# Optimization experiments

Measured on AMD Instinct MI355X. Metric: run time of the kernel, lower is better.

The kernel has to match this reference:

```python
import jax, jax.numpy as jnp
import numpy as np


def setup_inputs() -> dict:
    key = jax.random.key(0)
    kx, ks = jax.random.split(key)
    M, N, D = 8192, 8192, 512
    X = jax.random.normal(kx, (M, D), dtype=jnp.float32)
    svs = jax.random.normal(ks, (N, D), dtype=jnp.float32)
    # scale = 1/(2*sigma^2); a plausible fitted value for standard-normal data
    scale = jnp.asarray(0.01, dtype=jnp.float32)
    return {"X": X, "svs": svs, "scale": scale}


def reference(X, svs, scale):
    N, D = svs.shape
    x2 = jnp.sum(X * X, axis=-1, keepdims=True)          # [M, 1]
    s2 = jnp.sum(svs * svs, axis=-1)                      # [N]
    dist2 = x2 + s2[None, :] - 2.0 * (X @ svs.T)          # [M, N]
    dist2 = jnp.maximum(dist2, 0.0)
    log_p = (jax.scipy.special.logsumexp(-scale * dist2, axis=-1)
             - jnp.log(jnp.asarray(N, dtype=X.dtype))
             + (D / 2) * jnp.log(scale / jnp.pi))
    return log_p
```

## Files before the change

kernel.cpp:

```cpp
#include <hip/hip_runtime.h>
#include <hip/hip_bf16.h>
#include <hip/hip_fp8.h>
#include <math.h>

typedef __attribute__((ext_vector_type(4))) int   int4v;
typedef __attribute__((ext_vector_type(8))) int   int8v;
typedef __attribute__((ext_vector_type(4))) float f32x4;

#define AS1 __attribute__((address_space(1)))
#define AS3 __attribute__((address_space(3)))

__global__ __launch_bounds__(256) void prep_kernel(
    const float* __restrict__ X, const float* __restrict__ S,
    unsigned char* __restrict__ Xq, unsigned char* __restrict__ Sq,
    float* __restrict__ x2, float* __restrict__ s2,
    float* __restrict__ rowsum, int M, int R, int Dv)
{
    const int gid  = blockIdx.x * 256 + threadIdx.x;
    const int nthr = gridDim.x * 256;

    for (int i = gid; i < M; i += nthr) rowsum[i] = 0.f;

    const int lane = threadIdx.x & 63;
    const int wid  = gid >> 6;
    const int nw   = nthr >> 6;

    for (int row = wid; row < R; row += nw) {
        const float* rp;
        unsigned char* op;
        float* sq;
        if (row < M) { rp = X + (size_t)row * Dv;       op = Xq + (size_t)row * Dv;       sq = x2 + row; }
        else         { rp = S + (size_t)(row - M) * Dv; op = Sq + (size_t)(row - M) * Dv; sq = s2 + (row - M); }

        float acc = 0.f;
        for (int k = lane * 8; k < Dv; k += 64 * 8) {
            float4 v0 = *(const float4*)(rp + k);
            float4 v1 = *(const float4*)(rp + k + 4);
            acc += v0.x * v0.x + v0.y * v0.y + v0.z * v0.z + v0.w * v0.w;
            acc += v1.x * v1.x + v1.y * v1.y + v1.z * v1.z + v1.w * v1.w;
            union { __hip_fp8_e4m3 h[8]; uint2 u; } pk;
            pk.h[0] = __hip_fp8_e4m3(v0.x);
            pk.h[1] = __hip_fp8_e4m3(v0.y);
            pk.h[2] = __hip_fp8_e4m3(v0.z);
            pk.h[3] = __hip_fp8_e4m3(v0.w);
            pk.h[4] = __hip_fp8_e4m3(v1.x);
            pk.h[5] = __hip_fp8_e4m3(v1.y);
            pk.h[6] = __hip_fp8_e4m3(v1.z);
            pk.h[7] = __hip_fp8_e4m3(v1.w);
            *(uint2*)(op + k) = pk.u;
        }
#pragma unroll
        for (int off = 1; off < 64; off <<= 1)
            acc += __shfl_xor(acc, off, 64);
        if (lane == 0) *sq = acc;
    }
}

__global__ __launch_bounds__(256, 2) void kde_gemm512(
    const unsigned char* __restrict__ Xq,
    const unsigned char* __restrict__ Sq,
    const float* __restrict__ x2,
    const float* __restrict__ s2,
    const float* __restrict__ scale_p,
    float* __restrict__ rowsum,
    int M, int N)
{
    __shared__ char smem[65536];

    const int tid  = threadIdx.x;
    const int wave = tid >> 6;
    const int lane = tid & 63;
    const int quad = lane >> 4;
    const int l16  = lane & 15;

    const int m0 = blockIdx.x * 128;
    const int n0 = blockIdx.y * 128;
    const int wm = (wave & 1) * 64;
    const int wn = (wave >> 1) * 64;

    const float sc = *scale_p;

    f32x4 acc[4][4] = {};

    const int srow0 = wave * 8 + (lane >> 3);
    const int cg    = (lane & 7) ^ (lane >> 3);
    const unsigned char* gA = Xq + (size_t)(m0 + srow0) * 512 + cg * 16;
    const unsigned char* gB = Sq + (size_t)(n0 + srow0) * 512 + cg * 16;

#pragma unroll
    for (int rd = 0; rd < 4; ++rd)
        __builtin_amdgcn_global_load_lds(
            (const AS1 void*)(gA + (size_t)rd * 32 * 512),
            (AS3 void*)(smem + rd * 4096 + wave * 1024), 16, 0, 0);
#pragma unroll
    for (int rd = 0; rd < 4; ++rd)
        __builtin_amdgcn_global_load_lds(
            (const AS1 void*)(gB + (size_t)rd * 32 * 512),
            (AS3 void*)(smem + 16384 + rd * 4096 + wave * 1024), 16, 0, 0);

    const int e = l16 & 7;

#pragma unroll
    for (int k = 0; k < 4; ++k) {
        __syncthreads();

        if (k < 3) {
            const int k1 = (k + 1) * 128;
            char* dst = smem + ((k + 1) & 1) * 32768;
#pragma unroll
            for (int rd = 0; rd < 4; ++rd)
                __builtin_amdgcn_global_load_lds(
                    (const AS1 void*)(gA + (size_t)rd * 32 * 512 + k1),
                    (AS3 void*)(dst + rd * 4096 + wave * 1024), 16, 0, 0);
#pragma unroll
            for (int rd = 0; rd < 4; ++rd)
                __builtin_amdgcn_global_load_lds(
                    (const AS1 void*)(gB + (size_t)rd * 32 * 512 + k1),
                    (AS3 void*)(dst + 16384 + rd * 4096 + wave * 1024), 16, 0, 0);
        }

        const unsigned char* As = (const unsigned char*)(smem + (k & 1) * 32768);
        const unsigned char* Bs = As + 16384;

        int8v a_frag[4], b_frag[4];
#pragma unroll
        for (int mi = 0; mi < 4; ++mi) {
            const unsigned char* rowp = As + (wm + mi * 16 + l16) * 128;
            int4v lo = *(const int4v*)(rowp + ((2 * quad)     ^ e) * 16);
            int4v hi = *(const int4v*)(rowp + ((2 * quad + 1) ^ e) * 16);
            a_frag[mi] = (int8v){lo.x, lo.y, lo.z, lo.w, hi.x, hi.y, hi.z, hi.w};
        }
#pragma unroll
        for (int ni = 0; ni < 4; ++ni) {
            const unsigned char* rowp = Bs + (wn + ni * 16 + l16) * 128;
            int4v lo = *(const int4v*)(rowp + ((2 * quad)     ^ e) * 16);
            int4v hi = *(const int4v*)(rowp + ((2 * quad + 1) ^ e) * 16);
            b_frag[ni] = (int8v){lo.x, lo.y, lo.z, lo.w, hi.x, hi.y, hi.z, hi.w};
        }
#pragma unroll
        for (int mi = 0; mi < 4; ++mi)
#pragma unroll
            for (int ni = 0; ni < 4; ++ni)
                acc[mi][ni] = __builtin_amdgcn_mfma_scale_f32_16x16x128_f8f6f4(
                    a_frag[mi], b_frag[ni], acc[mi][ni],
                    0, 0, 0, 0x7F7F7F7F, 0, 0x7F7F7F7F);
    }

    __syncthreads();
    float* wred = (float*)smem + wave * (64 * 20);

    float s2v[4];
#pragma unroll
    for (int ni = 0; ni < 4; ++ni)
        s2v[ni] = s2[n0 + wn + ni * 16 + l16];

#pragma unroll
    for (int mi = 0; mi < 4; ++mi) {
#pragma unroll
        for (int r = 0; r < 4; ++r) {
            const int rowL = mi * 16 + quad * 4 + r;
            const float xv = x2[m0 + wm + rowL];
            float sum = 0.f;
#pragma unroll
            for (int ni = 0; ni < 4; ++ni) {
                float d2 = xv + s2v[ni] - 2.0f * acc[mi][ni][r];
                d2 = fmaxf(d2, 0.f);
                sum += __expf(-sc * d2);
            }
            wred[rowL * 20 + l16] = sum;
        }
    }
    __syncthreads();

    float4 p0 = *(float4*)(wred + lane * 20 + 0);
    float4 p1 = *(float4*)(wred + lane * 20 + 4);
    float4 p2 = *(float4*)(wred + lane * 20 + 8);
    float4 p3 = *(float4*)(wred + lane * 20 + 12);
    float s = (p0.x + p0.y + p0.z + p0.w) + (p1.x + p1.y + p1.z + p1.w)
            + (p2.x + p2.y + p2.z + p2.w) + (p3.x + p3.y + p3.z + p3.w);
    atomicAdd(&rowsum[m0 + wm + lane], s);
}

__global__ __launch_bounds__(256, 3) void kde_gemm_generic(
    const unsigned char* __restrict__ Xq, const unsigned char* __restrict__ Sq,
    const float* __restrict__ x2, const float* __restrict__ s2,
    const float* __restrict__ scale_p, float* __restrict__ rowsum,
    int M, int N, int Dv)
{
    const int D = Dv;
    __shared__ char smem[32768];
    unsigned char* As = (unsigned char*)smem;
    unsigned char* Bs = (unsigned char*)(smem + 16384);

    const int tid  = threadIdx.x;
    const int wave = tid >> 6;
    const int lane = tid & 63;
    const int quad = lane >> 4;
    const int l16  = lane & 15;

    const int m0 = blockIdx.x * 128;
    const int n0 = blockIdx.y * 128;
    const int wm = (wave & 1) * 64;
    const int wn = (wave >> 1) * 64;

    const float sc = *scale_p;
    f32x4 acc[4][4] = {};

    const int srow0 = wave * 8 + (lane >> 3);
    const int cg    = (lane & 7) ^ (lane >> 3);
    const unsigned char* gA = Xq + (size_t)(m0 + srow0) * D + cg * 16;
    const unsigned char* gB = Sq + (size_t)(n0 + srow0) * D + cg * 16;

    for (int k0 = 0; k0 < D; k0 += 128) {
        __syncthreads();
#pragma unroll
        for (int rd = 0; rd < 4; ++rd)
            __builtin_amdgcn_global_load_lds(
                (const AS1 void*)(gA + (size_t)rd * 32 * D + k0),
                (AS3 void*)(smem + rd * 4096 + wave * 1024), 16, 0, 0);
#pragma unroll
        for (int rd = 0; rd < 4; ++rd)
            __builtin_amdgcn_global_load_lds(
                (const AS1 void*)(gB + (size_t)rd * 32 * D + k0),
                (AS3 void*)(smem + 16384 + rd * 4096 + wave * 1024), 16, 0, 0);
        __syncthreads();

        const int e = l16 & 7;
        int8v a_frag[4], b_frag[4];
#pragma unroll
        for (int mi = 0; mi < 4; ++mi) {
            const unsigned char* rowp = As + (wm + mi * 16 + l16) * 128;
            int4v lo = *(const int4v*)(rowp + ((2 * quad)     ^ e) * 16);
            int4v hi = *(const int4v*)(rowp + ((2 * quad + 1) ^ e) * 16);
            a_frag[mi] = (int8v){lo.x, lo.y, lo.z, lo.w, hi.x, hi.y, hi.z, hi.w};
        }
#pragma unroll
        for (int ni = 0; ni < 4; ++ni) {
            const unsigned char* rowp = Bs + (wn + ni * 16 + l16) * 128;
            int4v lo = *(const int4v*)(rowp + ((2 * quad)     ^ e) * 16);
            int4v hi = *(const int4v*)(rowp + ((2 * quad + 1) ^ e) * 16);
            b_frag[ni] = (int8v){lo.x, lo.y, lo.z, lo.w, hi.x, hi.y, hi.z, hi.w};
        }
#pragma unroll
        for (int mi = 0; mi < 4; ++mi)
#pragma unroll
            for (int ni = 0; ni < 4; ++ni)
                acc[mi][ni] = __builtin_amdgcn_mfma_scale_f32_16x16x128_f8f6f4(
                    a_frag[mi], b_frag[ni], acc[mi][ni],
                    0, 0, 0, 0x7F7F7F7F, 0, 0x7F7F7F7F);
    }

    __syncthreads();
    float* wred = (float*)smem + wave * (64 * 20);

    float s2v[4];
#pragma unroll
    for (int ni = 0; ni < 4; ++ni)
        s2v[ni] = s2[n0 + wn + ni * 16 + l16];

#pragma unroll
    for (int mi = 0; mi < 4; ++mi) {
#pragma unroll
        for (int r = 0; r < 4; ++r) {
            const int rowL = mi * 16 + quad * 4 + r;
            const float xv = x2[m0 + wm + rowL];
            float sum = 0.f;
#pragma unroll
            for (int ni = 0; ni < 4; ++ni) {
                float d2 = xv + s2v[ni] - 2.0f * acc[mi][ni][r];
                d2 = fmaxf(d2, 0.f);
                sum += __expf(-sc * d2);
            }
            wred[rowL * 20 + l16] = sum;
        }
    }
    __syncthreads();

    float4 p0 = *(float4*)(wred + lane * 20 + 0);
    float4 p1 = *(float4*)(wred + lane * 20 + 4);
    float4 p2 = *(float4*)(wred + lane * 20 + 8);
    float4 p3 = *(float4*)(wred + lane * 20 + 12);
    float s = (p0.x + p0.y + p0.z + p0.w) + (p1.x + p1.y + p1.z + p1.w)
            + (p2.x + p2.y + p2.z + p2.w) + (p3.x + p3.y + p3.z + p3.w);
    atomicAdd(&rowsum[m0 + wm + lane], s);
}

__global__ void finalize_kernel(const float* __restrict__ rowsum,
                                const float* __restrict__ scale_p,
                                float* __restrict__ out, int M, int N, int Dv) {
    const int m = blockIdx.x * 256 + threadIdx.x;
    if (m < M) {
        const float sc = *scale_p;
        const float cst = -logf((float)N) + 0.5f * (float)Dv * logf(sc / 3.14159265358979f);
        out[m] = logf(rowsum[m]) + cst;
    }
}

extern "C" void kernel_launch(void* const* d_in, const int* in_sizes, int n_in,
                              void* d_out, int out_size, void* d_ws, size_t ws_size,
                              hipStream_t stream) {
    const float* X       = (const float*)d_in[0];
    const float* S       = (const float*)d_in[1];
    const float* scale_p = (const float*)d_in[2];
    float* out = (float*)d_out;

    const int M  = out_size;
    const int Dv = in_sizes[0] / M;
    const int N  = in_sizes[1] / Dv;

    char* ws = (char*)d_ws;
    unsigned char* Xq = (unsigned char*)ws;
    unsigned char* Sq = (unsigned char*)(ws + (size_t)M * Dv);
    float* x2     = (float*)(ws + (size_t)M * Dv + (size_t)N * Dv);
    float* s2     = x2 + M;
    float* rowsum = s2 + N;

    prep_kernel<<<512, 256, 0, stream>>>(X, S, Xq, Sq, x2, s2, rowsum, M, M + N, Dv);

    dim3 grid(M / 128, N / 128);
    if (Dv == 512)
        kde_gemm512<<<grid, 256, 0, stream>>>(Xq, Sq, x2, s2, scale_p, rowsum, M, N);
    else
        kde_gemm_generic<<<grid, 256, 0, stream>>>(Xq, Sq, x2, s2, scale_p, rowsum, M, N, Dv);

    finalize_kernel<<<(M + 255) / 256, 256, 0, stream>>>(rowsum, scale_p, out, M, N, Dv);
}
```

Baseline: 123.5 us.

## Retile fp8 KDE GEMM to 64x256 blocks with register-resident B fragments

The D=512 kernel changes from 128x128 tiles with double-buffered LDS staging of both operands to 64x256 tiles. The full 64x512 X tile is loaded into LDS once, and each wave streams its own S rows directly from global memory into registers, prefetching one K-chunk ahead. This removes the per-K-step barriers and the LDS traffic for B, halves LDS use, and raises the occupancy hint to 3 blocks. The cost is no reuse of B across waves (each S row is read by only one wave per block) and more global traffic for B, plus more atomics because the M tile is smaller.

```diff
diff --git a/kernel.cpp b/kernel.cpp
--- a/kernel.cpp
+++ b/kernel.cpp
@@ -56,7 +56,7 @@
     }
 }
 
-__global__ __launch_bounds__(256, 2) void kde_gemm512(
+__global__ __launch_bounds__(256, 3) void kde_gemm512(
     const unsigned char* __restrict__ Xq,
     const unsigned char* __restrict__ Sq,
     const float* __restrict__ x2,
@@ -65,7 +65,7 @@
     float* __restrict__ rowsum,
     int M, int N)
 {
-    __shared__ char smem[65536];
+    __shared__ char smem[32768];
 
     const int tid  = threadIdx.x;
     const int wave = tid >> 6;
@@ -73,76 +73,64 @@
     const int quad = lane >> 4;
     const int l16  = lane & 15;
 
-    const int m0 = blockIdx.x * 128;
-    const int n0 = blockIdx.y * 128;
-    const int wm = (wave & 1) * 64;
-    const int wn = (wave >> 1) * 64;
+    const int m0 = blockIdx.x * 64;
+    const int n0 = blockIdx.y * 256;
+    const int wn = wave * 64;
 
     const float sc = *scale_p;
 
+    const int srow = tid >> 5;
+    const int cg   = (tid & 31) ^ srow;
+    const unsigned char* gA = Xq + (size_t)(m0 + srow) * 512 + cg * 16;
+#pragma unroll
+    for (int r = 0; r < 8; ++r)
+        __builtin_amdgcn_global_load_lds(
+            (const AS1 void*)(gA + (size_t)r * 8 * 512),
+            (AS3 void*)(smem + r * 4096 + wave * 1024), 16, 0, 0);
+
+    const unsigned char* gBf = Sq + (size_t)(n0 + wn + l16) * 512 + quad * 32;
+    int4v blo[4], bhi[4];
+#pragma unroll
+    for (int ni = 0; ni < 4; ++ni) {
+        blo[ni] = *(const int4v*)(gBf + (size_t)ni * 16 * 512);
+        bhi[ni] = *(const int4v*)(gBf + (size_t)ni * 16 * 512 + 16);
+    }
+
     f32x4 acc[4][4] = {};
 
-    const int srow0 = wave * 8 + (lane >> 3);
-    const int cg    = (lane & 7) ^ (lane >> 3);
-    const unsigned char* gA = Xq + (size_t)(m0 + srow0) * 512 + cg * 16;
-    const unsigned char* gB = Sq + (size_t)(n0 + srow0) * 512 + cg * 16;
-
-#pragma unroll
-    for (int rd = 0; rd < 4; ++rd)
-        __builtin_amdgcn_global_load_lds(
-            (const AS1 void*)(gA + (size_t)rd * 32 * 512),
-            (AS3 void*)(smem + rd * 4096 + wave * 1024), 16, 0, 0);
-#pragma unroll
-    for (int rd = 0; rd < 4; ++rd)
-        __builtin_amdgcn_global_load_lds(
-            (const AS1 void*)(gB + (size_t)rd * 32 * 512),
-            (AS3 void*)(smem + 16384 + rd * 4096 + wave * 1024), 16, 0, 0);
+    __syncthreads();
 
     const int e = l16 & 7;
-
-#pragma unroll
-    for (int k = 0; k < 4; ++k) {
-        __syncthreads();
-
-        if (k < 3) {
-            const int k1 = (k + 1) * 128;
-            char* dst = smem + ((k + 1) & 1) * 32768;
-#pragma unroll
-            for (int rd = 0; rd < 4; ++rd)
-                __builtin_amdgcn_global_load_lds(
-                    (const AS1 void*)(gA + (size_t)rd * 32 * 512 + k1),
-                    (AS3 void*)(dst + rd * 4096 + wave * 1024), 16, 0, 0);
-#pragma unroll
-            for (int rd = 0; rd < 4; ++rd)
-                __builtin_amdgcn_global_load_lds(
-                    (const AS1 void*)(gB + (size_t)rd * 32 * 512 + k1),
-                    (AS3 void*)(dst + 16384 + rd * 4096 + wave * 1024), 16, 0, 0);
-        }
-
-        const unsigned char* As = (const unsigned char*)(smem + (k & 1) * 32768);
-        const unsigned char* Bs = As + 16384;
-
-        int8v a_frag[4], b_frag[4];
+    const unsigned char* As = (const unsigned char*)smem;
+
+#pragma unroll
+    for (int c = 0; c < 4; ++c) {
+        int8v bf[4];
+#pragma unroll
+        for (int ni = 0; ni < 4; ++ni)
+            bf[ni] = (int8v){blo[ni].x, blo[ni].y, blo[ni].z, blo[ni].w,
+                             bhi[ni].x, bhi[ni].y, bhi[ni].z, bhi[ni].w};
+        if (c < 3) {
+#pragma unroll
+            for (int ni = 0; ni < 4; ++ni) {
+                blo[ni] = *(const int4v*)(gBf + (size_t)ni * 16 * 512 + (c + 1) * 128);
+                bhi[ni] = *(const int4v*)(gBf + (size_t)ni * 16 * 512 + (c + 1) * 128 + 16);
+            }
+        }
+        int8v af[4];
 #pragma unroll
         for (int mi = 0; mi < 4; ++mi) {
-            const unsigned char* rowp = As + (wm + mi * 16 + l16) * 128;
-            int4v lo = *(const int4v*)(rowp + ((2 * quad)     ^ e) * 16);
-            int4v hi = *(const int4v*)(rowp + ((2 * quad + 1) ^ e) * 16);
-            a_frag[mi] = (int8v){lo.x, lo.y, lo.z, lo.w, hi.x, hi.y, hi.z, hi.w};
-        }
-#pragma unroll
-        for (int ni = 0; ni < 4; ++ni) {
-            const unsigned char* rowp = Bs + (wn + ni * 16 + l16) * 128;
-            int4v lo = *(const int4v*)(rowp + ((2 * quad)     ^ e) * 16);
-            int4v hi = *(const int4v*)(rowp + ((2 * quad + 1) ^ e) * 16);
-            b_frag[ni] = (int8v){lo.x, lo.y, lo.z, lo.w, hi.x, hi.y, hi.z, hi.w};
+            const unsigned char* rowp = As + (size_t)(mi * 16 + l16) * 512;
+            int4v lo = *(const int4v*)(rowp + ((8 * c + 2 * quad)     ^ e) * 16);
+            int4v hi = *(const int4v*)(rowp + ((8 * c + 2 * quad + 1) ^ e) * 16);
+            af[mi] = (int8v){lo.x, lo.y, lo.z, lo.w, hi.x, hi.y, hi.z, hi.w};
         }
 #pragma unroll
         for (int mi = 0; mi < 4; ++mi)
 #pragma unroll
             for (int ni = 0; ni < 4; ++ni)
                 acc[mi][ni] = __builtin_amdgcn_mfma_scale_f32_16x16x128_f8f6f4(
-                    a_frag[mi], b_frag[ni], acc[mi][ni],
+                    af[mi], bf[ni], acc[mi][ni],
                     0, 0, 0, 0x7F7F7F7F, 0, 0x7F7F7F7F);
     }
 
@@ -159,7 +147,7 @@
 #pragma unroll
         for (int r = 0; r < 4; ++r) {
             const int rowL = mi * 16 + quad * 4 + r;
-            const float xv = x2[m0 + wm + rowL];
+            const float xv = x2[m0 + rowL];
             float sum = 0.f;
 #pragma unroll
             for (int ni = 0; ni < 4; ++ni) {
@@ -172,13 +160,14 @@
     }
     __syncthreads();
 
-    float4 p0 = *(float4*)(wred + lane * 20 + 0);
-    float4 p1 = *(float4*)(wred + lane * 20 + 4);
-    float4 p2 = *(float4*)(wred + lane * 20 + 8);
-    float4 p3 = *(float4*)(wred + lane * 20 + 12);
+    float* rp = wred + lane * 20;
+    float4 p0 = *(float4*)(rp + 0);
+    float4 p1 = *(float4*)(rp + 4);
+    float4 p2 = *(float4*)(rp + 8);
+    float4 p3 = *(float4*)(rp + 12);
     float s = (p0.x + p0.y + p0.z + p0.w) + (p1.x + p1.y + p1.z + p1.w)
             + (p2.x + p2.y + p2.z + p2.w) + (p3.x + p3.y + p3.z + p3.w);
-    atomicAdd(&rowsum[m0 + wm + lane], s);
+    atomicAdd(&rowsum[m0 + lane], s);
 }
 
 __global__ __launch_bounds__(256, 3) void kde_gemm_generic(
@@ -317,11 +306,13 @@
 
     prep_kernel<<<512, 256, 0, stream>>>(X, S, Xq, Sq, x2, s2, rowsum, M, M + N, Dv);
 
-    dim3 grid(M / 128, N / 128);
-    if (Dv == 512)
+    if (Dv == 512) {
+        dim3 grid(M / 64, N / 256);
         kde_gemm512<<<grid, 256, 0, stream>>>(Xq, Sq, x2, s2, scale_p, rowsum, M, N);
-    else
+    } else {
+        dim3 grid(M / 128, N / 128);
         kde_gemm_generic<<<grid, 256, 0, stream>>>(Xq, Sq, x2, s2, scale_p, rowsum, M, N, Dv);
+    }
 
     finalize_kernel<<<(M + 255) / 256, 256, 0, stream>>>(rowsum, scale_p, out, M, N, Dv);
 }
```

Result: slower. 158.1 us (+28.0%).

## Enlarge GEMM block tile to 256x128 with 8 waves, drop double buffering

Applied to the files above, without the earlier changes.

The Dv=512 kernel now uses 512-thread blocks covering 256 rows of X by 128 rows of svs, so each block reuses its B tile across twice as many rows and the grid is halved. The double-buffered async LDS prefetch is replaced by a single 48KB buffer with load, sync and compute per K step. This cuts LDS per block so more blocks can be resident, relying on occupancy to hide load latency instead of in-block prefetch. The risk is exposed global-to-LDS latency on each of the four K steps.

```diff
diff --git a/kernel.cpp b/kernel.cpp
--- a/kernel.cpp
+++ b/kernel.cpp
@@ -56,7 +56,7 @@
     }
 }
 
-__global__ __launch_bounds__(256, 2) void kde_gemm512(
+__global__ __launch_bounds__(512, 4) void kde_gemm512(
     const unsigned char* __restrict__ Xq,
     const unsigned char* __restrict__ Sq,
     const float* __restrict__ x2,
@@ -65,7 +65,9 @@
     float* __restrict__ rowsum,
     int M, int N)
 {
-    __shared__ char smem[65536];
+    __shared__ char smem[49152];
+    unsigned char* As = (unsigned char*)smem;
+    unsigned char* Bs = (unsigned char*)(smem + 32768);
 
     const int tid  = threadIdx.x;
     const int wave = tid >> 6;
@@ -73,66 +75,47 @@
     const int quad = lane >> 4;
     const int l16  = lane & 15;
 
-    const int m0 = blockIdx.x * 128;
+    const int m0 = blockIdx.x * 256;
     const int n0 = blockIdx.y * 128;
-    const int wm = (wave & 1) * 64;
-    const int wn = (wave >> 1) * 64;
+    const int wm = (wave >> 1) * 64;
+    const int wn = (wave & 1) * 64;
 
     const float sc = *scale_p;
 
     f32x4 acc[4][4] = {};
 
-    const int srow0 = wave * 8 + (lane >> 3);
-    const int cg    = (lane & 7) ^ (lane >> 3);
-    const unsigned char* gA = Xq + (size_t)(m0 + srow0) * 512 + cg * 16;
-    const unsigned char* gB = Sq + (size_t)(n0 + srow0) * 512 + cg * 16;
-
-#pragma unroll
-    for (int rd = 0; rd < 4; ++rd)
-        __builtin_amdgcn_global_load_lds(
-            (const AS1 void*)(gA + (size_t)rd * 32 * 512),
-            (AS3 void*)(smem + rd * 4096 + wave * 1024), 16, 0, 0);
-#pragma unroll
-    for (int rd = 0; rd < 4; ++rd)
-        __builtin_amdgcn_global_load_lds(
-            (const AS1 void*)(gB + (size_t)rd * 32 * 512),
-            (AS3 void*)(smem + 16384 + rd * 4096 + wave * 1024), 16, 0, 0);
-
-    const int e = l16 & 7;
-
-#pragma unroll
-    for (int k = 0; k < 4; ++k) {
+    const int srow = tid >> 3;
+    const int cg   = (tid & 7) ^ (srow & 7);
+    const unsigned char* gA = Xq + (size_t)(m0 + srow) * 512 + cg * 16;
+    const unsigned char* gB = Sq + (size_t)(n0 + srow) * 512 + cg * 16;
+
+#pragma unroll
+    for (int k0 = 0; k0 < 512; k0 += 128) {
         __syncthreads();
-
-        if (k < 3) {
-            const int k1 = (k + 1) * 128;
-            char* dst = smem + ((k + 1) & 1) * 32768;
-#pragma unroll
-            for (int rd = 0; rd < 4; ++rd)
-                __builtin_amdgcn_global_load_lds(
-                    (const AS1 void*)(gA + (size_t)rd * 32 * 512 + k1),
-                    (AS3 void*)(dst + rd * 4096 + wave * 1024), 16, 0, 0);
-#pragma unroll
-            for (int rd = 0; rd < 4; ++rd)
-                __builtin_amdgcn_global_load_lds(
-                    (const AS1 void*)(gB + (size_t)rd * 32 * 512 + k1),
-                    (AS3 void*)(dst + 16384 + rd * 4096 + wave * 1024), 16, 0, 0);
-        }
-
-        const unsigned char* As = (const unsigned char*)(smem + (k & 1) * 32768);
-        const unsigned char* Bs = As + 16384;
-
+#pragma unroll
+        for (int rd = 0; rd < 4; ++rd)
+            __builtin_amdgcn_global_load_lds(
+                (const AS1 void*)(gA + (size_t)rd * 64 * 512 + k0),
+                (AS3 void*)(smem + rd * 8192 + wave * 1024), 16, 0, 0);
+#pragma unroll
+        for (int rd = 0; rd < 2; ++rd)
+            __builtin_amdgcn_global_load_lds(
+                (const AS1 void*)(gB + (size_t)rd * 64 * 512 + k0),
+                (AS3 void*)(smem + 32768 + rd * 8192 + wave * 1024), 16, 0, 0);
+        __syncthreads();
+
+        const int e = l16 & 7;
         int8v a_frag[4], b_frag[4];
 #pragma unroll
         for (int mi = 0; mi < 4; ++mi) {
-            const unsigned char* rowp = As + (wm + mi * 16 + l16) * 128;
+            const unsigned char* rowp = As + (size_t)(wm + mi * 16 + l16) * 128;
             int4v lo = *(const int4v*)(rowp + ((2 * quad)     ^ e) * 16);
             int4v hi = *(const int4v*)(rowp + ((2 * quad + 1) ^ e) * 16);
             a_frag[mi] = (int8v){lo.x, lo.y, lo.z, lo.w, hi.x, hi.y, hi.z, hi.w};
         }
 #pragma unroll
         for (int ni = 0; ni < 4; ++ni) {
-            const unsigned char* rowp = Bs + (wn + ni * 16 + l16) * 128;
+            const unsigned char* rowp = Bs + (size_t)(wn + ni * 16 + l16) * 128;
             int4v lo = *(const int4v*)(rowp + ((2 * quad)     ^ e) * 16);
             int4v hi = *(const int4v*)(rowp + ((2 * quad + 1) ^ e) * 16);
             b_frag[ni] = (int8v){lo.x, lo.y, lo.z, lo.w, hi.x, hi.y, hi.z, hi.w};
@@ -147,7 +130,7 @@
     }
 
     __syncthreads();
-    float* wred = (float*)smem + wave * (64 * 20);
+    float* wred = (float*)(smem + wave * 5120);
 
     float s2v[4];
 #pragma unroll
@@ -172,10 +155,11 @@
     }
     __syncthreads();
 
-    float4 p0 = *(float4*)(wred + lane * 20 + 0);
-    float4 p1 = *(float4*)(wred + lane * 20 + 4);
-    float4 p2 = *(float4*)(wred + lane * 20 + 8);
-    float4 p3 = *(float4*)(wred + lane * 20 + 12);
+    float* rp = wred + lane * 20;
+    float4 p0 = *(float4*)(rp + 0);
+    float4 p1 = *(float4*)(rp + 4);
+    float4 p2 = *(float4*)(rp + 8);
+    float4 p3 = *(float4*)(rp + 12);
     float s = (p0.x + p0.y + p0.z + p0.w) + (p1.x + p1.y + p1.z + p1.w)
             + (p2.x + p2.y + p2.z + p2.w) + (p3.x + p3.y + p3.z + p3.w);
     atomicAdd(&rowsum[m0 + wm + lane], s);
@@ -317,11 +301,13 @@
 
     prep_kernel<<<512, 256, 0, stream>>>(X, S, Xq, Sq, x2, s2, rowsum, M, M + N, Dv);
 
-    dim3 grid(M / 128, N / 128);
-    if (Dv == 512)
-        kde_gemm512<<<grid, 256, 0, stream>>>(Xq, Sq, x2, s2, scale_p, rowsum, M, N);
-    else
+    if (Dv == 512 && (M % 256) == 0 && (N % 128) == 0) {
+        dim3 grid(M / 256, N / 128);
+        kde_gemm512<<<grid, 512, 0, stream>>>(Xq, Sq, x2, s2, scale_p, rowsum, M, N);
+    } else {
+        dim3 grid(M / 128, N / 128);
         kde_gemm_generic<<<grid, 256, 0, stream>>>(Xq, Sq, x2, s2, scale_p, rowsum, M, N, Dv);
+    }
 
     finalize_kernel<<<(M + 255) / 256, 256, 0, stream>>>(rowsum, scale_p, out, M, N, Dv);
 }
```

After: 149.6 us. 1.21x slower.
